# Kernel tuning notes

Measured on AMD Instinct MI355X. Metric: run time of the kernel, lower is better.

Reference implementation:

```python
import jax, jax.numpy as jnp
from jax import lax
import numpy as np

LOG2PI = float(np.log(2.0 * np.pi))
FMIN = float(np.finfo(np.float32).min)


def seq_mask(lengths, maxlen):
    # [B, maxlen] float32
    return (jnp.arange(maxlen)[None] < lengths[:, None]).astype(jnp.float32)


def monotonic_alignment_search(ll, attnmask):
    """Faithful port of GlowTTS.monotonic_alignment_search.
    ll, attnmask: [B, T, S] float32. Returns [B, T, S] float32.
    Note: replicates the source exactly, including stacking backtracked rows
    in descending-j (append) order before masking, as written in the TF code.
    """
    B, T, S = ll.shape
    x_range = jnp.arange(S)[None]  # [1, S]

    def fwd(prob, j_and_ll):
        j, ll_j = j_and_ll  # ll_j: [B, S]
        prev = jnp.pad(prob, ((0, 0), (1, 0)), constant_values=-jnp.inf)[:, :-1]
        max_mask = prob >= prev                       # [B, S] bool
        prob_max = jnp.where(max_mask, prob, prev)
        prob_new = jnp.where(x_range <= j, prob_max + ll_j, FMIN)
        return prob_new, max_mask

    _, direction = lax.scan(fwd, jnp.zeros((B, S), jnp.float32),
                            (jnp.arange(T), jnp.transpose(ll, (1, 0, 2))))
    direction = jnp.transpose(direction, (1, 0, 2)).astype(jnp.int32)  # [B, T, S]
    direction = jnp.where(attnmask.astype(bool), direction, 1)

    index = attnmask[:, 0].sum(axis=-1).astype(jnp.int32) - 1  # [B]
    brange = jnp.arange(B)

    def bwd(index, j):
        attn_j = jax.nn.one_hot(index, S, dtype=jnp.float32)  # drops index<0 like scatter_nd
        d = direction[brange, j, index]                       # [B]
        return index + d - 1, attn_j

    _, attn = lax.scan(bwd, index, jnp.arange(T)[::-1])
    attn = jnp.transpose(attn, (1, 0, 2))  # [B, T, S], rows in append order
    return attn * attnmask


def setup_inputs() -> dict:
    key = jax.random.key(0)
    k1, k2, k3, k4, k5 = jax.random.split(key, 5)
    B, T, S, C = 32, 1200, 384, 160
    latent = jax.random.normal(k1, (B, T, C), dtype=jnp.float32)
    mean = jax.random.normal(k2, (B, S, C), dtype=jnp.float32)
    logdur = jax.random.normal(k3, (B, S), dtype=jnp.float32)
    textlen = jax.random.randint(k4, (B,), S // 2, S + 1).astype(jnp.int32)
    mellen = jax.random.randint(k5, (B,), T // 2, T + 1).astype(jnp.int32)
    return {"latent": latent, "mean": mean, "logdur": logdur,
            "textlen": textlen, "mellen": mellen}


def reference(latent, mean, logdur, textlen, mellen):
    B, T, C = latent.shape
    S = mean.shape[1]
    mask = seq_mask(textlen, S)     # [B, S]
    melmask = seq_mask(mellen, T)   # [B, T]
    attnmask = melmask[..., None] * mask[:, None]  # [B, T, S]

    # pairwise squared distance (cdist via matmul + reduce_sum)
    dist = (jnp.sum(jnp.square(latent), axis=-1, keepdims=True)
            - 2.0 * jnp.einsum('btc,bsc->bts', latent, mean)
            + jnp.sum(jnp.square(mean), axis=-1)[:, None])
    ll = -0.5 * (LOG2PI + dist) * attnmask

    attn = lax.stop_gradient(monotonic_alignment_search(ll, attnmask))
    aligned = jnp.einsum('bts,bsc->btc', attn, mean)  # [B, T, C]

    # negative log-likelihood (dlogdet of the flow omitted: constant here)
    nll = 0.5 * (LOG2PI + jnp.sum(jnp.square(latent - aligned), axis=(1, 2)))
    nll = jnp.mean(nll / (mellen * C).astype(jnp.float32))

    gtdur = jnp.log(jnp.maximum(jnp.sum(attn, axis=1), 1e-05)) * mask
    durloss = jnp.sum(jnp.square(logdur - gtdur), axis=-1) / mellen.astype(jnp.float32)
    durloss = jnp.mean(durloss)

    loss = nll + durloss
    return loss, attn
```

## Files before the change

kernel.cpp:

```cpp
#include <hip/hip_runtime.h>
#include <math.h>

#define LOG2PI 1.8378770664093453f
#define F32MIN (-3.4028234663852886e38f)
#define SMAX 384
#define RST 388
#define NW 38

__global__ __launch_bounds__(64) void k_sums(
    const float* __restrict__ latent, const float* __restrict__ mean,
    float* __restrict__ lx2, float* __restrict__ lm2, int BT, int BS, int C) {
  int row = blockIdx.x;
  int lane = threadIdx.x;
  const float* src;
  float* dst;
  if (row < BT) { src = latent + (size_t)row * C; dst = lx2 + row; }
  else          { src = mean + (size_t)(row - BT) * C; dst = lm2 + (row - BT); }
  float s = 0.f;
  for (int c = lane; c < C; c += 64) { float v = src[c]; s += v * v; }
  #pragma unroll
  for (int off = 32; off; off >>= 1) s += __shfl_down(s, off);
  if (lane == 0) *dst = s;
}

__global__ __launch_bounds__(256) void k_scores(
    const float* __restrict__ latent, const float* __restrict__ mean,
    const float* __restrict__ lx2, const float* __restrict__ lm2,
    const int* __restrict__ textlen, const int* __restrict__ mellen,
    float* __restrict__ ll, int T, int S, int C) {
  int b  = blockIdx.z;
  int t0 = blockIdx.x * 64;
  int s0 = blockIdx.y * 64;
  int mel = mellen[b], txt = textlen[b];
  int tid = threadIdx.x;
  int ty = tid >> 4, tx = tid & 15;
  float* out = ll + ((size_t)b * T + t0) * S + s0;

  if (t0 >= mel || s0 >= txt || s0 > t0 + 63) return;

  __shared__ float At[16][64];
  __shared__ float Bt[16][64];
  float acc[4][4] = {};

  const float* Ab = latent + ((size_t)b * T + t0) * C;
  const float* Bb = mean + ((size_t)b * S + s0) * C;

  for (int kk = 0; kk < C; kk += 16) {
    int r  = tid >> 2;
    int cg = tid & 3;
    float4 a = (t0 + r < T) ? *(const float4*)(Ab + (size_t)r * C + kk + cg * 4)
                            : make_float4(0.f, 0.f, 0.f, 0.f);
    float4 bm = *(const float4*)(Bb + (size_t)r * C + kk + cg * 4);
    At[cg * 4 + 0][r] = a.x;  At[cg * 4 + 1][r] = a.y;
    At[cg * 4 + 2][r] = a.z;  At[cg * 4 + 3][r] = a.w;
    Bt[cg * 4 + 0][r] = bm.x; Bt[cg * 4 + 1][r] = bm.y;
    Bt[cg * 4 + 2][r] = bm.z; Bt[cg * 4 + 3][r] = bm.w;
    __syncthreads();
    #pragma unroll
    for (int k = 0; k < 16; ++k) {
      float4 a4 = *(const float4*)&At[k][ty * 4];
      float4 b4 = *(const float4*)&Bt[k][tx * 4];
      float av[4] = {a4.x, a4.y, a4.z, a4.w};
      float bv[4] = {b4.x, b4.y, b4.z, b4.w};
      #pragma unroll
      for (int i = 0; i < 4; ++i)
        #pragma unroll
        for (int j = 0; j < 4; ++j)
          acc[i][j] = fmaf(av[i], bv[j], acc[i][j]);
    }
    __syncthreads();
  }

  #pragma unroll
  for (int i = 0; i < 4; ++i) {
    int t = t0 + ty * 4 + i;
    if (t >= T) continue;
    float lx = lx2[(size_t)b * T + t];
    float4 o;
    float* po = &o.x;
    #pragma unroll
    for (int j = 0; j < 4; ++j) {
      int s = s0 + tx * 4 + j;
      float d = lx - 2.f * acc[i][j] + lm2[(size_t)b * S + s];
      float v = -0.5f * (LOG2PI + d);
      po[j] = (t < mel && s < txt) ? v : 0.f;
    }
    *(float4*)(out + (size_t)(ty * 4 + i) * S + tx * 4) = o;
  }
}

__device__ __forceinline__ float dpp_shr1_neginf(float x) {
  int r = __builtin_amdgcn_update_dpp(
      __float_as_int(-INFINITY), __float_as_int(x),
      0x138 , 0xf, 0xf, false);
  return __int_as_float(r);
}

template <bool MASKED>
__device__ __forceinline__ void mas_step(
    int t, int sbase, int r, const float2 A0, const float2 A1, const float2 A2,
    float& p0, float& p1, float& p2, float& p3, float& p4, float& p5,
    unsigned& n0, unsigned& n1, unsigned& n2, unsigned& n3, unsigned& n4,
    unsigned& n5) {
  float l0 = A0.x, l1 = A0.y, l2 = A1.x, l3 = A1.y, l4 = A2.x, l5 = A2.y;
  float pm1 = dpp_shr1_neginf(p5);
  unsigned s0b = __float_as_uint(p0 - pm1) >> 31;
  unsigned s1b = __float_as_uint(p1 - p0)  >> 31;
  unsigned s2b = __float_as_uint(p2 - p1)  >> 31;
  unsigned s3b = __float_as_uint(p3 - p2)  >> 31;
  unsigned s4b = __float_as_uint(p4 - p3)  >> 31;
  unsigned s5b = __float_as_uint(p5 - p4)  >> 31;
  n0 |= s0b << r; n1 |= s1b << r; n2 |= s2b << r;
  n3 |= s3b << r; n4 |= s4b << r; n5 |= s5b << r;
  float v0 = fmaxf(p0, pm1) + l0;
  float v1 = fmaxf(p1, p0) + l1;
  float v2 = fmaxf(p2, p1) + l2;
  float v3 = fmaxf(p3, p2) + l3;
  float v4 = fmaxf(p4, p3) + l4;
  float v5 = fmaxf(p5, p4) + l5;
  if (MASKED) {
    p0 = (sbase + 0 <= t) ? v0 : F32MIN;
    p1 = (sbase + 1 <= t) ? v1 : F32MIN;
    p2 = (sbase + 2 <= t) ? v2 : F32MIN;
    p3 = (sbase + 3 <= t) ? v3 : F32MIN;
    p4 = (sbase + 4 <= t) ? v4 : F32MIN;
    p5 = (sbase + 5 <= t) ? v5 : F32MIN;
  } else {
    p0 = v0; p1 = v1; p2 = v2; p3 = v3; p4 = v4; p5 = v5;
  }
}

template <bool MASKED, int ROWS>
__device__ __forceinline__ void scan_chunk_lds(
    const float* __restrict__ rcur, int t0, int sbase,
    float& p0, float& p1, float& p2, float& p3, float& p4, float& p5,
    unsigned* __restrict__ dirT, int cw) {
  unsigned n0 = 0, n1 = 0, n2 = 0, n3 = 0, n4 = 0, n5 = 0;
  const float2* q = (const float2*)(rcur + sbase);
  float2 A0 = q[0], A1 = q[1], A2 = q[2];
  #pragma unroll 1
  for (int r = 0; r < ROWS; r += 2) {
    const float2* qb = q + (size_t)(r + 1) * (RST / 2);
    float2 B0 = qb[0], B1 = qb[1], B2 = qb[2];
    mas_step<MASKED>(t0 + r, sbase, r, A0, A1, A2,
                     p0, p1, p2, p3, p4, p5, n0, n1, n2, n3, n4, n5);
    int rn = (r + 2 < ROWS) ? (r + 2) : (ROWS - 1);
    const float2* qa = q + (size_t)rn * (RST / 2);
    A0 = qa[0]; A1 = qa[1]; A2 = qa[2];
    mas_step<MASKED>(t0 + r + 1, sbase, r + 1, B0, B1, B2,
                     p0, p1, p2, p3, p4, p5, n0, n1, n2, n3, n4, n5);
  }
  unsigned* dcol = dirT + (unsigned)sbase * NW + cw;
  dcol[0] = ~n0; dcol[NW] = ~n1; dcol[2 * NW] = ~n2;
  dcol[3 * NW] = ~n3; dcol[4 * NW] = ~n4; dcol[5 * NW] = ~n5;
}

__global__ __launch_bounds__(256, 1) void k_scan(
    const float* __restrict__ ll, const int* __restrict__ textlen,
    const int* __restrict__ mellen, int* __restrict__ pathidx, int T, int S) {
  int b = blockIdx.x;
  int tid = threadIdx.x;
  int lane = tid & 63;
  __shared__ float rows[2][32][RST];
  __shared__ unsigned dirT[SMAX * NW];

  const float* llb = ll + (size_t)b * T * S;
  int mel = mellen[b], txt = textlen[b];
  int sbase = lane * 6;
  int nfull = T / 32;
  int nch = (T + 31) / 32;
  int nchb = (mel + 31) / 32;
  if (nchb > nch) nchb = nch;
  float p0 = 0.f, p1 = 0.f, p2 = 0.f, p3 = 0.f, p4 = 0.f, p5 = 0.f;

  if (tid >= 64) {
    int lid = tid - 64;
    const float4* g = (const float4*)llb;
    #pragma unroll
    for (int k = 0; k < 16; ++k) {
      int f = k * 192 + lid;
      ((float4*)&rows[0][f / 96][0])[f % 96] = g[f];
    }
  }
  __syncthreads();

  for (int c = 0; c < nchb; ++c) {
    if (tid >= 64) {
      int nxt = c + 1;
      if (nxt < nchb) {
        int lid = tid - 64;
        const float4* g = (const float4*)(llb + (size_t)nxt * 32 * S);
        if (nxt < nfull) {
          float4 stg[16];
          #pragma unroll
          for (int k = 0; k < 16; ++k) stg[k] = g[k * 192 + lid];
          #pragma unroll
          for (int k = 0; k < 16; ++k) {
            int f = k * 192 + lid;
            ((float4*)&rows[nxt & 1][f / 96][0])[f % 96] = stg[k];
          }
        } else {
          float4 stg[8];
          #pragma unroll
          for (int k = 0; k < 8; ++k) stg[k] = g[k * 192 + lid];
          #pragma unroll
          for (int k = 0; k < 8; ++k) {
            int f = k * 192 + lid;
            ((float4*)&rows[nxt & 1][f / 96][0])[f % 96] = stg[k];
          }
        }
      }
    } else {
      const float* rc = &rows[c & 1][0][0];
      int t0 = c * 32;
      if (c < 12)
        scan_chunk_lds<true, 32>(rc, t0, sbase, p0, p1, p2, p3, p4, p5, dirT, c);
      else if (c < nfull)
        scan_chunk_lds<false, 32>(rc, t0, sbase, p0, p1, p2, p3, p4, p5, dirT, c);
      else
        scan_chunk_lds<false, 16>(rc, t0, sbase, p0, p1, p2, p3, p4, p5, dirT, c);
    }
    __syncthreads();
  }

  if (tid >= 64) return;

  size_t base = (size_t)b * T;
  int k0 = T - mel;
  for (int k = lane; k < k0; k += 64) pathidx[base + k] = txt - 1;

  if (lane == 0) {
    int i = txt - 1;
    int j = mel - 1;
    unsigned w = ~0u;
    bool reload = true;
    for (int k = k0; k < T; ++k) {
      pathidx[base + k] = i;
      if (reload) {
        int ii = (i < 0) ? i + S : i;
        ii = (ii < 0) ? 0 : ii;
        w = (ii < txt) ? dirT[ii * NW + (j >> 5)] : ~0u;
      }
      int d = (int)((w >> (j & 31)) & 1u);
      reload = (d == 0) | ((j & 31) == 0);
      i += d - 1;
      --j;
    }
  }
}

__global__ __launch_bounds__(256) void k_scatter(
    float* __restrict__ attn, const int* __restrict__ pathidx,
    const int* __restrict__ textlen, const int* __restrict__ mellen,
    int B, int T, int S) {
  size_t idx = ((size_t)blockIdx.x * blockDim.x + threadIdx.x) * 4;
  size_t total = (size_t)B * T * S;
  if (idx >= total) return;
  int s = (int)(idx % S);
  size_t row = idx / S;
  int b = (int)(row / T);
  int k = (int)(row % T);
  int pi = pathidx[row];
  int mel = mellen[b], txt = textlen[b];
  float4 o = make_float4(0.f, 0.f, 0.f, 0.f);
  if (k < mel && pi >= 0 && pi < S && pi < txt && pi >= s && pi < s + 4)
    (&o.x)[pi - s] = 1.f;
  *(float4*)(attn + idx) = o;
}

__global__ __launch_bounds__(256) void k_rowloss(
    const float* __restrict__ latent, const float* __restrict__ mean,
    const int* __restrict__ pathidx, const int* __restrict__ textlen,
    const int* __restrict__ mellen, float* __restrict__ rowsum,
    int T, int S, int C) {
  int row = blockIdx.x * 4 + (threadIdx.x >> 6);
  int lane = threadIdx.x & 63;
  int b = row / T, k = row % T;
  int pi = pathidx[row];
  int mel = mellen[b], txt = textlen[b];
  bool on = (k < mel) && (pi >= 0) && (pi < S) && (pi < txt);
  const float* L = latent + (size_t)row * C;
  const float* M = mean + ((size_t)b * S + (on ? pi : 0)) * C;
  float s = 0.f;
  for (int c = lane; c < C; c += 64) {
    float d = L[c] - (on ? M[c] : 0.f);
    s += d * d;
  }
  #pragma unroll
  for (int off = 32; off; off >>= 1) s += __shfl_down(s, off);
  if (lane == 0) rowsum[row] = s;
}

__global__ __launch_bounds__(256) void k_batch(
    const float* __restrict__ rowsum, const int* __restrict__ pathidx,
    const float* __restrict__ logdur, const int* __restrict__ textlen,
    const int* __restrict__ mellen, float* __restrict__ nllc,
    float* __restrict__ durc, int T, int S, int C) {
  int b = blockIdx.x;
  int tid = threadIdx.x;
  __shared__ int hist[512];
  __shared__ float red[256];
  int mel = mellen[b], txt = textlen[b];
  for (int s = tid; s < S; s += 256) hist[s] = 0;
  __syncthreads();
  for (int k = tid; k < T; k += 256) {
    int pi = pathidx[(size_t)b * T + k];
    if (k < mel && pi >= 0 && pi < S && pi < txt) atomicAdd(&hist[pi], 1);
  }
  __syncthreads();
  float part = 0.f;
  for (int s = tid; s < S; s += 256) {
    float cnt = (float)hist[s];
    float gt = logf(fmaxf(cnt, 1e-5f));
    gt = (s < txt) ? gt : 0.f;
    float d = logdur[(size_t)b * S + s] - gt;
    part += d * d;
  }
  red[tid] = part; __syncthreads();
  #pragma unroll
  for (int off = 128; off; off >>= 1) {
    if (tid < off) red[tid] += red[tid + off];
    __syncthreads();
  }
  if (tid == 0) durc[b] = red[0] / (float)mel;
  __syncthreads();
  part = 0.f;
  for (int k = tid; k < T; k += 256) part += rowsum[(size_t)b * T + k];
  red[tid] = part; __syncthreads();
  #pragma unroll
  for (int off = 128; off; off >>= 1) {
    if (tid < off) red[tid] += red[tid + off];
    __syncthreads();
  }
  if (tid == 0) nllc[b] = 0.5f * (LOG2PI + red[0]) / ((float)mel * (float)C);
}

__global__ __launch_bounds__(64) void k_final(
    const float* __restrict__ nllc, const float* __restrict__ durc,
    float* __restrict__ out, int B) {
  int lane = threadIdx.x;
  float v = (lane < B) ? (nllc[lane] + durc[lane]) : 0.f;
  #pragma unroll
  for (int off = 32; off; off >>= 1) v += __shfl_down(v, off);
  if (lane == 0) out[0] = v / (float)B;
}

extern "C" void kernel_launch(void* const* d_in, const int* in_sizes, int n_in,
                              void* d_out, int out_size, void* d_ws, size_t ws_size,
                              hipStream_t stream) {
  (void)n_in; (void)out_size; (void)ws_size;
  const float* latent = (const float*)d_in[0];
  const float* mean   = (const float*)d_in[1];
  const float* logdur = (const float*)d_in[2];
  const int*   textlen = (const int*)d_in[3];
  const int*   mellen  = (const int*)d_in[4];

  int B = in_sizes[3];
  int S = in_sizes[2] / B;
  int C = in_sizes[1] / (B * S);
  int T = in_sizes[0] / (B * C);

  float* out = (float*)d_out;
  float* ll = out + 1;

  char* ws = (char*)d_ws;
  float* lx2    = (float*)ws;
  float* lm2    = lx2 + (size_t)B * T;
  int*   pathidx = (int*)(lm2 + (size_t)B * S);
  float* rowsum  = (float*)(pathidx + (size_t)B * T);
  float* nllc    = rowsum + (size_t)B * T;
  float* durc    = nllc + B;

  k_sums<<<B * T + B * S, 64, 0, stream>>>(latent, mean, lx2, lm2, B * T, B * S, C);

  dim3 g2((T + 63) / 64, (S + 63) / 64, B);
  k_scores<<<g2, 256, 0, stream>>>(latent, mean, lx2, lm2, textlen, mellen, ll, T, S, C);

  k_scan<<<B, 256, 0, stream>>>(ll, textlen, mellen, pathidx, T, S);

  size_t total = (size_t)B * T * S;
  k_scatter<<<(int)((total / 4 + 255) / 256), 256, 0, stream>>>(ll, pathidx, textlen, mellen, B, T, S);

  k_rowloss<<<(B * T) / 4, 256, 0, stream>>>(latent, mean, pathidx, textlen, mellen, rowsum, T, S, C);

  k_batch<<<B, 256, 0, stream>>>(rowsum, pathidx, logdur, textlen, mellen, nllc, durc, T, S, C);

  k_final<<<1, 64, 0, stream>>>(nllc, durc, out, B);
}
```

Measured before the change: 321.1 us.

## Enlarge score GEMM tiles to 128x128, unpad scan LDS rows, bitmask row masking

The score GEMM now uses 128x128 output tiles with an 8x8 per-thread register tile and a k-step of 8, raising arithmetic intensity and cutting global reloads of latent and mean. The scan kernel drops the padded LDS row stride (388 to 384), so staging becomes flat contiguous float4 copies with no per-element index math. The masked DP step uses integer bitmask selects in place of compare-and-select. The trade-offs are more registers per thread in the GEMM, coarser tile-level early-exit skipping, and possible LDS bank conflicts from removing the padding.

```diff
diff --git a/kernel.cpp b/kernel.cpp
--- a/kernel.cpp
+++ b/kernel.cpp
@@ -4,7 +4,6 @@
 #define LOG2PI 1.8378770664093453f
 #define F32MIN (-3.4028234663852886e38f)
 #define SMAX 384
-#define RST 388
 #define NW 38
 
 __global__ __launch_bounds__(64) void k_sums(
@@ -29,63 +28,68 @@
     const int* __restrict__ textlen, const int* __restrict__ mellen,
     float* __restrict__ ll, int T, int S, int C) {
   int b  = blockIdx.z;
-  int t0 = blockIdx.x * 64;
-  int s0 = blockIdx.y * 64;
-  int mel = mellen[b], txt = textlen[b];
+  int t0 = blockIdx.x * 128;
+  int s0 = blockIdx.y * 128;
+  int mel = mellen[b], txt = textlen[b];
+  if (t0 >= mel || s0 >= txt || s0 > t0 + 127) return;
+
   int tid = threadIdx.x;
   int ty = tid >> 4, tx = tid & 15;
-  float* out = ll + ((size_t)b * T + t0) * S + s0;
-
-  if (t0 >= mel || s0 >= txt || s0 > t0 + 63) return;
-
-  __shared__ float At[16][64];
-  __shared__ float Bt[16][64];
-  float acc[4][4] = {};
+  int lrow = tid >> 1, lcg = tid & 1;
+
+  __shared__ float At[8][128];
+  __shared__ float Bt[8][128];
+  float acc[8][8] = {};
 
   const float* Ab = latent + ((size_t)b * T + t0) * C;
   const float* Bb = mean + ((size_t)b * S + s0) * C;
 
-  for (int kk = 0; kk < C; kk += 16) {
-    int r  = tid >> 2;
-    int cg = tid & 3;
-    float4 a = (t0 + r < T) ? *(const float4*)(Ab + (size_t)r * C + kk + cg * 4)
-                            : make_float4(0.f, 0.f, 0.f, 0.f);
-    float4 bm = *(const float4*)(Bb + (size_t)r * C + kk + cg * 4);
-    At[cg * 4 + 0][r] = a.x;  At[cg * 4 + 1][r] = a.y;
-    At[cg * 4 + 2][r] = a.z;  At[cg * 4 + 3][r] = a.w;
-    Bt[cg * 4 + 0][r] = bm.x; Bt[cg * 4 + 1][r] = bm.y;
-    Bt[cg * 4 + 2][r] = bm.z; Bt[cg * 4 + 3][r] = bm.w;
+  for (int kk = 0; kk < C; kk += 8) {
+    float4 a = (t0 + lrow < T)
+                   ? *(const float4*)(Ab + (size_t)lrow * C + kk + lcg * 4)
+                   : make_float4(0.f, 0.f, 0.f, 0.f);
+    float4 bm = *(const float4*)(Bb + (size_t)lrow * C + kk + lcg * 4);
+    __syncthreads();
+    At[lcg * 4 + 0][lrow] = a.x;  At[lcg * 4 + 1][lrow] = a.y;
+    At[lcg * 4 + 2][lrow] = a.z;  At[lcg * 4 + 3][lrow] = a.w;
+    Bt[lcg * 4 + 0][lrow] = bm.x; Bt[lcg * 4 + 1][lrow] = bm.y;
+    Bt[lcg * 4 + 2][lrow] = bm.z; Bt[lcg * 4 + 3][lrow] = bm.w;
     __syncthreads();
     #pragma unroll
-    for (int k = 0; k < 16; ++k) {
-      float4 a4 = *(const float4*)&At[k][ty * 4];
-      float4 b4 = *(const float4*)&Bt[k][tx * 4];
-      float av[4] = {a4.x, a4.y, a4.z, a4.w};
-      float bv[4] = {b4.x, b4.y, b4.z, b4.w};
+    for (int k = 0; k < 8; ++k) {
+      float4 a0 = *(const float4*)&At[k][ty * 8];
+      float4 a1 = *(const float4*)&At[k][ty * 8 + 4];
+      float4 b0 = *(const float4*)&Bt[k][tx * 8];
+      float4 b1 = *(const float4*)&Bt[k][tx * 8 + 4];
+      float av[8] = {a0.x, a0.y, a0.z, a0.w, a1.x, a1.y, a1.z, a1.w};
+      float bv[8] = {b0.x, b0.y, b0.z, b0.w, b1.x, b1.y, b1.z, b1.w};
       #pragma unroll
-      for (int i = 0; i < 4; ++i)
+      for (int i = 0; i < 8; ++i)
         #pragma unroll
-        for (int j = 0; j < 4; ++j)
+        for (int j = 0; j < 8; ++j)
           acc[i][j] = fmaf(av[i], bv[j], acc[i][j]);
     }
-    __syncthreads();
-  }
-
-  #pragma unroll
-  for (int i = 0; i < 4; ++i) {
-    int t = t0 + ty * 4 + i;
+  }
+
+  #pragma unroll
+  for (int i = 0; i < 8; ++i) {
+    int t = t0 + ty * 8 + i;
     if (t >= T) continue;
     float lx = lx2[(size_t)b * T + t];
-    float4 o;
-    float* po = &o.x;
+    bool trow = t < mel;
+    float* out = ll + ((size_t)b * T + t) * S + s0 + tx * 8;
+    float4 o0, o1;
+    float* po = &o0.x;
     #pragma unroll
-    for (int j = 0; j < 4; ++j) {
-      int s = s0 + tx * 4 + j;
+    for (int j = 0; j < 8; ++j) {
+      if (j == 4) po = &o1.x;
+      int s = s0 + tx * 8 + j;
       float d = lx - 2.f * acc[i][j] + lm2[(size_t)b * S + s];
       float v = -0.5f * (LOG2PI + d);
-      po[j] = (t < mel && s < txt) ? v : 0.f;
+      po[j & 3] = (trow && s < txt) ? v : 0.f;
     }
-    *(float4*)(out + (size_t)(ty * 4 + i) * S + tx * 4) = o;
+    *(float4*)out = o0;
+    *(float4*)(out + 4) = o1;
   }
 }
 
@@ -94,6 +98,10 @@
       __float_as_int(-INFINITY), __float_as_int(x),
       0x138 , 0xf, 0xf, false);
   return __int_as_float(r);
+}
+
+__device__ __forceinline__ float selmask(float v, int m) {
+  return __int_as_float((__float_as_int(v) & ~m) | ((int)0xFF7FFFFF & m));
 }
 
 template <bool MASKED>
@@ -119,12 +127,13 @@
   float v4 = fmaxf(p4, p3) + l4;
   float v5 = fmaxf(p5, p4) + l5;
   if (MASKED) {
-    p0 = (sbase + 0 <= t) ? v0 : F32MIN;
-    p1 = (sbase + 1 <= t) ? v1 : F32MIN;
-    p2 = (sbase + 2 <= t) ? v2 : F32MIN;
-    p3 = (sbase + 3 <= t) ? v3 : F32MIN;
-    p4 = (sbase + 4 <= t) ? v4 : F32MIN;
-    p5 = (sbase + 5 <= t) ? v5 : F32MIN;
+    int base = t - sbase;
+    p0 = selmask(v0, (base - 0) >> 31);
+    p1 = selmask(v1, (base - 1) >> 31);
+    p2 = selmask(v2, (base - 2) >> 31);
+    p3 = selmask(v3, (base - 3) >> 31);
+    p4 = selmask(v4, (base - 4) >> 31);
+    p5 = selmask(v5, (base - 5) >> 31);
   } else {
     p0 = v0; p1 = v1; p2 = v2; p3 = v3; p4 = v4; p5 = v5;
   }
@@ -140,12 +149,12 @@
   float2 A0 = q[0], A1 = q[1], A2 = q[2];
   #pragma unroll 1
   for (int r = 0; r < ROWS; r += 2) {
-    const float2* qb = q + (size_t)(r + 1) * (RST / 2);
+    const float2* qb = q + (size_t)(r + 1) * 192;
     float2 B0 = qb[0], B1 = qb[1], B2 = qb[2];
     mas_step<MASKED>(t0 + r, sbase, r, A0, A1, A2,
                      p0, p1, p2, p3, p4, p5, n0, n1, n2, n3, n4, n5);
     int rn = (r + 2 < ROWS) ? (r + 2) : (ROWS - 1);
-    const float2* qa = q + (size_t)rn * (RST / 2);
+    const float2* qa = q + (size_t)rn * 192;
     A0 = qa[0]; A1 = qa[1]; A2 = qa[2];
     mas_step<MASKED>(t0 + r + 1, sbase, r + 1, B0, B1, B2,
                      p0, p1, p2, p3, p4, p5, n0, n1, n2, n3, n4, n5);
@@ -161,7 +170,7 @@
   int b = blockIdx.x;
   int tid = threadIdx.x;
   int lane = tid & 63;
-  __shared__ float rows[2][32][RST];
+  __shared__ float rows[2][32][SMAX];
   __shared__ unsigned dirT[SMAX * NW];
 
   const float* llb = ll + (size_t)b * T * S;
@@ -176,11 +185,9 @@
   if (tid >= 64) {
     int lid = tid - 64;
     const float4* g = (const float4*)llb;
+    float4* d = (float4*)&rows[0][0][0];
     #pragma unroll
-    for (int k = 0; k < 16; ++k) {
-      int f = k * 192 + lid;
-      ((float4*)&rows[0][f / 96][0])[f % 96] = g[f];
-    }
+    for (int k = 0; k < 16; ++k) d[k * 192 + lid] = g[k * 192 + lid];
   }
   __syncthreads();
 
@@ -190,24 +197,19 @@
       if (nxt < nchb) {
         int lid = tid - 64;
         const float4* g = (const float4*)(llb + (size_t)nxt * 32 * S);
+        float4* d = (float4*)&rows[nxt & 1][0][0];
         if (nxt < nfull) {
           float4 stg[16];
           #pragma unroll
           for (int k = 0; k < 16; ++k) stg[k] = g[k * 192 + lid];
           #pragma unroll
-          for (int k = 0; k < 16; ++k) {
-            int f = k * 192 + lid;
-            ((float4*)&rows[nxt & 1][f / 96][0])[f % 96] = stg[k];
-          }
+          for (int k = 0; k < 16; ++k) d[k * 192 + lid] = stg[k];
         } else {
           float4 stg[8];
           #pragma unroll
           for (int k = 0; k < 8; ++k) stg[k] = g[k * 192 + lid];
           #pragma unroll
-          for (int k = 0; k < 8; ++k) {
-            int f = k * 192 + lid;
-            ((float4*)&rows[nxt & 1][f / 96][0])[f % 96] = stg[k];
-          }
+          for (int k = 0; k < 8; ++k) d[k * 192 + lid] = stg[k];
         }
       }
     } else {
@@ -373,7 +375,7 @@
 
   k_sums<<<B * T + B * S, 64, 0, stream>>>(latent, mean, lx2, lm2, B * T, B * S, C);
 
-  dim3 g2((T + 63) / 64, (S + 63) / 64, B);
+  dim3 g2((T + 127) / 128, (S + 127) / 128, B);
   k_scores<<<g2, 256, 0, stream>>>(latent, mean, lx2, lm2, textlen, mellen, ll, T, S, C);
 
   k_scan<<<B, 256, 0, stream>>>(ll, textlen, mellen, pathidx, T, S);
```

Result: slower. 339.6 us (+5.8%).
